# Kernel optimization log

Hardware: AMD Instinct MI355X
Metric: run time of the kernel (lower is better)

Reference implementation:

```python
import jax, jax.numpy as jnp
import numpy as np

D_MODEL = 1024
NUM_HEADS = 16
D_K = D_MODEL // NUM_HEADS


def setup_inputs() -> dict:
    key = jax.random.key(0)
    ks = jax.random.split(key, 8)
    B, S = 2, 2048
    query = jax.random.normal(ks[0], (B, S, D_MODEL), dtype=jnp.float32)
    k_in = jax.random.normal(ks[1], (B, S, D_MODEL), dtype=jnp.float32)
    value = jax.random.normal(ks[2], (B, S, D_MODEL), dtype=jnp.float32)
    # causal mask: True = masked out (upper triangle above diagonal)
    mask = jnp.triu(jnp.ones((S, S), dtype=bool), k=1)[None, None, :, :]
    scale = 1.0 / np.sqrt(D_MODEL)
    W_q = jax.random.normal(ks[3], (D_MODEL, D_MODEL), dtype=jnp.float32) * scale
    W_k = jax.random.normal(ks[4], (D_MODEL, D_MODEL), dtype=jnp.float32) * scale
    W_v = jax.random.normal(ks[5], (D_MODEL, D_MODEL), dtype=jnp.float32) * scale
    W_o = jax.random.normal(ks[6], (D_MODEL, D_MODEL), dtype=jnp.float32) * scale
    return {"query": query, "key": k_in, "value": value, "mask": mask,
            "W_q": W_q, "W_k": W_k, "W_v": W_v, "W_o": W_o}


def _split(x):
    # [B, S, d_model] -> [B, h, S, d_k]
    B, S, _ = x.shape
    return x.reshape(B, S, NUM_HEADS, D_K).transpose(0, 2, 1, 3)


def reference(query, key, value, mask, W_q, W_k, W_v, W_o):
    # torch nn.Linear(bias=False): y = x @ W.T
    Q = _split(query @ W_q.T)   # [B, h, Sq, d_k]
    K = _split(key @ W_k.T)     # [B, h, Sk, d_k]
    V = _split(value @ W_v.T)   # [B, h, Sk, d_k]
    scores = jnp.einsum('bhqd,bhkd->bhqk', Q, K) / jnp.sqrt(jnp.float32(D_K))
    scores = jnp.where(mask, -jnp.inf, scores)
    attn_w = jax.nn.softmax(scores, axis=-1)
    attn_w = jnp.nan_to_num(attn_w, nan=0.0)
    out = jnp.einsum('bhqk,bhkd->bhqd', attn_w, V)  # [B, h, Sq, d_k]
    B, _, Sq, _ = out.shape
    merged = out.transpose(0, 2, 1, 3).reshape(B, Sq, D_MODEL)
    return merged @ W_o.T
```

## Files before the change

kernel.cpp:

```cpp
#include <hip/hip_runtime.h>
#include <hip/hip_bf16.h>
#include <stdint.h>

typedef __attribute__((ext_vector_type(4))) float f32x4;
typedef __attribute__((ext_vector_type(8))) __bf16 bf16x8;
typedef __attribute__((ext_vector_type(4))) unsigned short us4;

#define SEQ 2048
#define DMODEL 1024
#define NH 16
#define DK 64
#define MTOT 4096

__device__ __forceinline__ unsigned short f2bf(float x) {
  union { float f; unsigned int u; } v; v.f = x;
  unsigned int r = v.u + 0x7fffu + ((v.u >> 16) & 1u);
  return (unsigned short)(r >> 16);
}

__device__ __forceinline__ unsigned int cvtpk(float lo, float hi) {
  unsigned int r;
  asm("v_cvt_pk_bf16_f32 %0, %1, %2" : "=v"(r) : "v"(lo), "v"(hi));
  return r;
}

__device__ __forceinline__ f32x4 mfma_bf16(bf16x8 a, bf16x8 b, f32x4 c) {
  return __builtin_amdgcn_mfma_f32_16x16x32_bf16(a, b, c, 0, 0, 0);
}

__device__ __forceinline__ void gload16(const unsigned short* g, unsigned short* l) {
  __builtin_amdgcn_global_load_lds((__attribute__((address_space(1))) void*)g,
                                   (__attribute__((address_space(3))) void*)l,
                                   16, 0, 0);
}

__global__ void cvt_all(const float* __restrict__ s0, const float* __restrict__ s1,
                        const float* __restrict__ s2, const float* __restrict__ s3,
                        const float* __restrict__ s4, const float* __restrict__ s5,
                        const float* __restrict__ s6,
                        unsigned short* __restrict__ d0, unsigned short* __restrict__ d1,
                        unsigned short* __restrict__ d2, unsigned short* __restrict__ d3,
                        unsigned short* __restrict__ d4, unsigned short* __restrict__ d5,
                        unsigned short* __restrict__ d6) {
  const int y = blockIdx.y;
  const float* s = y == 0 ? s0 : y == 1 ? s1 : y == 2 ? s2 : y == 3 ? s3
                 : y == 4 ? s4 : y == 5 ? s5 : s6;
  unsigned short* d = y == 0 ? d0 : y == 1 ? d1 : y == 2 ? d2 : y == 3 ? d3
                    : y == 4 ? d4 : y == 5 ? d5 : d6;
  const int n4 = (y < 3) ? (MTOT * DMODEL / 4) : (DMODEL * DMODEL / 4);
  const int stride = gridDim.x * blockDim.x;
  for (int i = blockIdx.x * blockDim.x + threadIdx.x; i < n4; i += stride) {
    f32x4 v = reinterpret_cast<const f32x4*>(s)[i];
    us4 o;
    o.x = f2bf(v.x); o.y = f2bf(v.y); o.z = f2bf(v.z); o.w = f2bf(v.w);
    reinterpret_cast<us4*>(d)[i] = o;
  }
}

__global__ __launch_bounds__(256) void gemm_qkv(
    const unsigned short* __restrict__ xq, const unsigned short* __restrict__ xk,
    const unsigned short* __restrict__ xv, const unsigned short* __restrict__ bwq,
    const unsigned short* __restrict__ bwk, const unsigned short* __restrict__ bwv,
    unsigned short* __restrict__ Qh, unsigned short* __restrict__ Kh,
    unsigned short* __restrict__ Vt) {
  const int z = blockIdx.z;
  const unsigned short* A = z == 0 ? xq : (z == 1 ? xk : xv);
  const unsigned short* B = z == 0 ? bwq : (z == 1 ? bwk : bwv);
  const float scale = z == 0 ? 0.18033688011112042f : 1.0f;

  __shared__ __align__(16) unsigned short lA[128 * 32];
  __shared__ __align__(16) unsigned short lB[128 * 32];
  const int tid = threadIdx.x;
  const int lane = tid & 63;
  const int wid = tid >> 6;
  const int l15 = lane & 15, l4 = lane >> 4;
  const int bm = blockIdx.x, bn = blockIdx.y;
  const int wr = wid >> 1, wc = wid & 1;

  f32x4 acc[4][4] = {};

  const int chunk0 = (wid * 2 + 0) * 64 + lane;
  const int chunk1 = (wid * 2 + 1) * 64 + lane;
  const unsigned short* gA0 = A + (size_t)(bm * 128 + (chunk0 >> 2)) * 1024 + (chunk0 & 3) * 8;
  const unsigned short* gA1 = A + (size_t)(bm * 128 + (chunk1 >> 2)) * 1024 + (chunk1 & 3) * 8;
  const unsigned short* gB0 = B + (size_t)(bn * 128 + (chunk0 >> 2)) * 1024 + (chunk0 & 3) * 8;
  const unsigned short* gB1 = B + (size_t)(bn * 128 + (chunk1 >> 2)) * 1024 + (chunk1 & 3) * 8;
  unsigned short* lA0 = lA + (wid * 2 + 0) * 512;
  unsigned short* lA1 = lA + (wid * 2 + 1) * 512;
  unsigned short* lB0 = lB + (wid * 2 + 0) * 512;
  unsigned short* lB1 = lB + (wid * 2 + 1) * 512;

  for (int kt = 0; kt < 1024; kt += 32) {
    __syncthreads();
    gload16(gA0 + kt, lA0);
    gload16(gA1 + kt, lA1);
    gload16(gB0 + kt, lB0);
    gload16(gB1 + kt, lB1);
    __syncthreads();
    bf16x8 af[4], bfr[4];
#pragma unroll
    for (int i = 0; i < 4; ++i)
      af[i] = *reinterpret_cast<const bf16x8*>(&lA[(wr * 64 + i * 16 + l15) * 32 + l4 * 8]);
#pragma unroll
    for (int j = 0; j < 4; ++j)
      bfr[j] = *reinterpret_cast<const bf16x8*>(&lB[(wc * 64 + j * 16 + l15) * 32 + l4 * 8]);
    if (z < 2) {
#pragma unroll
      for (int i = 0; i < 4; ++i)
#pragma unroll
        for (int j = 0; j < 4; ++j)
          acc[i][j] = mfma_bf16(bfr[j], af[i], acc[i][j]);
    } else {
#pragma unroll
      for (int i = 0; i < 4; ++i)
#pragma unroll
        for (int j = 0; j < 4; ++j)
          acc[i][j] = mfma_bf16(af[i], bfr[j], acc[i][j]);
    }
  }

  const int row0 = bm * 128 + wr * 64;
  const int col0 = bn * 128 + wc * 64;

  if (z < 2) {
    unsigned short* out = z ? Kh : Qh;
#pragma unroll
    for (int i = 0; i < 4; ++i) {
      const int m = row0 + i * 16 + l15;
      const int b = m >> 11, s = m & 2047;
#pragma unroll
      for (int j = 0; j < 4; ++j) {
        const int n0 = col0 + j * 16 + l4 * 4;
        const int h = n0 >> 6, dd = n0 & 63;
        union { us4 h4; unsigned int u[2]; } pk;
        pk.u[0] = cvtpk(acc[i][j][0] * scale, acc[i][j][1] * scale);
        pk.u[1] = cvtpk(acc[i][j][2] * scale, acc[i][j][3] * scale);
        *reinterpret_cast<us4*>(&out[(size_t)(b * NH + h) * (SEQ * DK) + s * DK + dd]) = pk.h4;
      }
    }
  } else {
#pragma unroll
    for (int i = 0; i < 4; ++i) {
      const int m0 = row0 + i * 16 + l4 * 4;
      const int b = m0 >> 11, s0 = m0 & 2047;
      const int g = (s0 >> 2) & 7;
      const int col = (s0 & ~31) + ((g & 3) << 3) + ((g >> 2) << 2);
#pragma unroll
      for (int j = 0; j < 4; ++j) {
        const int n = col0 + j * 16 + l15;
        const int h = n >> 6, dd = n & 63;
        union { us4 h4; unsigned int u[2]; } pk;
        pk.u[0] = cvtpk(acc[i][j][0], acc[i][j][1]);
        pk.u[1] = cvtpk(acc[i][j][2], acc[i][j][3]);
        *reinterpret_cast<us4*>(&Vt[(size_t)(b * NH + h) * (DK * SEQ) + dd * SEQ + col]) = pk.h4;
      }
    }
  }
}

__global__ __launch_bounds__(512) void gemm_o(const unsigned short* __restrict__ A,
                                              const unsigned short* __restrict__ B,
                                              float* __restrict__ out) {
  __shared__ __align__(16) unsigned short lA3[3][128 * 64];
  __shared__ __align__(16) unsigned short lB3[3][128 * 64];

  const int tid = threadIdx.x;
  const int lane = tid & 63, wid = tid >> 6;
  const int l15 = lane & 15, l4 = lane >> 4;
  const int bm = blockIdx.x, bn = blockIdx.y;
  const int wr = wid >> 1, wc = wid & 1;

  f32x4 acc[2][4] = {};

  const int r8 = lane >> 3, c8 = lane & 7;
  const unsigned short* gAs[2];
  const unsigned short* gBs[2];
  int dstoff[2];
#pragma unroll
  for (int is = 0; is < 2; ++is) {
    const int rbase = is * 64 + wid * 8;
    gAs[is] = A + (size_t)(bm * 128 + rbase + r8) * 1024 + (c8 ^ r8) * 8;
    gBs[is] = B + (size_t)(bn * 128 + rbase + r8) * 1024 + (c8 ^ r8) * 8;
    dstoff[is] = rbase * 64;
  }

#define STAGE_O(t, buf)                                         \
  {                                                             \
    const int kb = (t) * 64;                                    \
    gload16(gAs[0] + kb, &lA3[buf][dstoff[0]]);                 \
    gload16(gAs[1] + kb, &lA3[buf][dstoff[1]]);                 \
    gload16(gBs[0] + kb, &lB3[buf][dstoff[0]]);                 \
    gload16(gBs[1] + kb, &lB3[buf][dstoff[1]]);                 \
  }

  STAGE_O(0, 0);
  STAGE_O(1, 1);

#pragma unroll 1
  for (int t = 0; t < 16; ++t) {
    if (t + 1 < 16) {
      asm volatile("s_waitcnt vmcnt(4)" ::: "memory");
    } else {
      asm volatile("s_waitcnt vmcnt(0)" ::: "memory");
    }
    __builtin_amdgcn_sched_barrier(0);
    __builtin_amdgcn_s_barrier();
    __builtin_amdgcn_sched_barrier(0);

    if (t + 2 < 16) {
      const int pb = (t + 2) % 3;
      STAGE_O(t + 2, pb);
    }

    const unsigned short* La = lA3[t % 3];
    const unsigned short* Lb = lB3[t % 3];
#pragma unroll
    for (int kk = 0; kk < 2; ++kk) {
      bf16x8 af[2], bf[4];
#pragma unroll
      for (int i = 0; i < 2; ++i) {
        const int row = wr * 32 + i * 16 + l15;
        af[i] = *reinterpret_cast<const bf16x8*>(
            &La[row * 64 + (((kk * 4 + l4) ^ (l15 & 7)) * 8)]);
      }
#pragma unroll
      for (int j = 0; j < 4; ++j) {
        const int row = wc * 64 + j * 16 + l15;
        bf[j] = *reinterpret_cast<const bf16x8*>(
            &Lb[row * 64 + (((kk * 4 + l4) ^ (l15 & 7)) * 8)]);
      }
#pragma unroll
      for (int i = 0; i < 2; ++i)
#pragma unroll
        for (int j = 0; j < 4; ++j)
          acc[i][j] = mfma_bf16(bf[j], af[i], acc[i][j]);
    }
  }
#undef STAGE_O

  const int row0 = bm * 128 + wr * 32;
  const int col0 = bn * 128 + wc * 64;
#pragma unroll
  for (int i = 0; i < 2; ++i) {
    const int m = row0 + i * 16 + l15;
#pragma unroll
    for (int j = 0; j < 4; ++j) {
      const int n0 = col0 + j * 16 + l4 * 4;
      *reinterpret_cast<f32x4*>(&out[(size_t)m * DMODEL + n0]) = acc[i][j];
    }
  }
}

__global__ __launch_bounds__(512, 2) void attn_kernel(const unsigned short* __restrict__ Qh,
                                                      const unsigned short* __restrict__ Kh,
                                                      const unsigned short* __restrict__ Vt,
                                                      unsigned short* __restrict__ Mg) {
  __shared__ __align__(16) unsigned short Kl[4][64 * 64];
  __shared__ __align__(16) unsigned short Vl[4][64 * 64];

  const int tid = threadIdx.x;
  const int lane = tid & 63;
  const int w = tid >> 6;
  const int l15 = lane & 15, l4 = lane >> 4;

  const int d = blockIdx.x;
  const int base = d & 255;
  const int pair = d >> 8;
  const int xcd = base & 7;
  const int jj = base >> 3;
  const int bh = (jj >> 3) * 8 + xcd;
  const int qi = jj & 7;
  const int tau = pair ? qi : 15 - qi;

  const unsigned short* Qb = Qh + (size_t)bh * SEQ * DK;
  const unsigned short* Kb = Kh + (size_t)bh * SEQ * DK;
  const unsigned short* Vb = Vt + (size_t)bh * DK * SEQ;
  const int bq = bh >> 4, hh = bh & 15;
  unsigned short* Mbase = Mg + (size_t)bq * SEQ * DMODEL + hh * DK;

  const int srow = lane >> 3;
  const int sswz = (lane & 7) ^ srow;
  const unsigned short* KsrcB = Kb + (size_t)(w * 8 + srow) * DK + sswz * 8;
  const unsigned short* VsrcB = Vb + (size_t)(w * 8 + srow) * SEQ + sswz * 8;

  const int l7 = l15 & 7;

  const int qbase = tau * 128;
  const int q0w = qbase + w * 16;
  const int nt = 2 * tau + 2;

  bf16x8 qf0 = *reinterpret_cast<const bf16x8*>(Qb + (size_t)(q0w + l15) * DK + l4 * 8);
  bf16x8 qf1 = *reinterpret_cast<const bf16x8*>(Qb + (size_t)(q0w + l15) * DK + 32 + l4 * 8);

  f32x4 o[4] = {};
  float mrow = -__builtin_inff();
  float lrow = 0.0f;

  gload16(KsrcB, &Kl[0][w * 512]);
  gload16(VsrcB, &Vl[0][w * 512]);
  gload16(KsrcB + (size_t)64 * DK, &Kl[1][w * 512]);
  gload16(VsrcB + 64, &Vl[1][w * 512]);

  const int S = nt >> 1;
#pragma unroll 1
  for (int s = 0; s < S; ++s) {
    const int t0 = s << 1;
    const int kbase0 = t0 << 6;

    asm volatile("s_waitcnt vmcnt(0)" ::: "memory");
    __builtin_amdgcn_sched_barrier(0);
    __builtin_amdgcn_s_barrier();
    __builtin_amdgcn_sched_barrier(0);

    if (t0 + 2 < nt) {
      gload16(KsrcB + (size_t)(kbase0 + 128) * DK, &Kl[(t0 + 2) & 3][w * 512]);
      gload16(VsrcB + (kbase0 + 128), &Vl[(t0 + 2) & 3][w * 512]);
      gload16(KsrcB + (size_t)(kbase0 + 192) * DK, &Kl[(t0 + 3) & 3][w * 512]);
      gload16(VsrcB + (kbase0 + 192), &Vl[(t0 + 3) & 3][w * 512]);
    }

#pragma unroll
    for (int u = 0; u < 2; ++u) {
      const int t = t0 + u;
      const int kbase = t << 6;
      if (kbase >= q0w + 16) continue;
      const unsigned short* Kc = Kl[t & 3];
      const unsigned short* Vc = Vl[t & 3];

      f32x4 sc[4];
      __builtin_amdgcn_s_setprio(1);
#pragma unroll
      for (int c = 0; c < 4; ++c) {
        const int krow = c * 16 + l15;
        bf16x8 kf0 = *reinterpret_cast<const bf16x8*>(&Kc[krow * 64 + ((l4 ^ l7) * 8)]);
        bf16x8 kf1 = *reinterpret_cast<const bf16x8*>(&Kc[krow * 64 + (((4 + l4) ^ l7) * 8)]);
        f32x4 z = {0.f, 0.f, 0.f, 0.f};
        z = mfma_bf16(kf0, qf0, z);
        sc[c] = mfma_bf16(kf1, qf1, z);
      }
      __builtin_amdgcn_s_setprio(0);

      if (kbase + 63 > q0w) {
        const int qg = q0w + l15;
#pragma unroll
        for (int c = 0; c < 4; ++c) {
          const int kp = kbase + c * 16 + l4 * 4;
#pragma unroll
          for (int r = 0; r < 4; ++r)
            if (kp + r > qg) sc[c][r] = -__builtin_inff();
        }
      }

      f32x4 mv = sc[0];
#pragma unroll
      for (int c = 1; c < 4; ++c)
#pragma unroll
        for (int r = 0; r < 4; ++r) mv[r] = fmaxf(mv[r], sc[c][r]);
      float pm = fmaxf(fmaxf(mv[0], mv[1]), fmaxf(mv[2], mv[3]));
      if (!__all(pm - mrow <= 8.0f)) {
        pm = fmaxf(pm, __shfl_xor(pm, 16));
        pm = fmaxf(pm, __shfl_xor(pm, 32));
        const float mn = fmaxf(mrow, pm);
        const float al = __builtin_amdgcn_exp2f(mrow - mn);
        mrow = mn;
        lrow *= al;
#pragma unroll
        for (int dd = 0; dd < 4; ++dd)
#pragma unroll
          for (int r = 0; r < 4; ++r) o[dd][r] *= al;
      }
      union PB { bf16x8 v; unsigned int u[4]; } pbv[2];
      f32x4 sv = {0.f, 0.f, 0.f, 0.f};
#pragma unroll
      for (int c = 0; c < 4; ++c) {
        const float p0 = __builtin_amdgcn_exp2f(sc[c][0] - mrow);
        const float p1 = __builtin_amdgcn_exp2f(sc[c][1] - mrow);
        const float p2 = __builtin_amdgcn_exp2f(sc[c][2] - mrow);
        const float p3 = __builtin_amdgcn_exp2f(sc[c][3] - mrow);
        sv[0] += p0; sv[1] += p1; sv[2] += p2; sv[3] += p3;
        pbv[c >> 1].u[(c & 1) * 2 + 0] = cvtpk(p0, p1);
        pbv[c >> 1].u[(c & 1) * 2 + 1] = cvtpk(p2, p3);
      }
      lrow += (sv[0] + sv[1]) + (sv[2] + sv[3]);

      __builtin_amdgcn_s_setprio(1);
#pragma unroll
      for (int dd = 0; dd < 4; ++dd) {
        const int vrow = dd * 16 + l15;
#pragma unroll
        for (int p = 0; p < 2; ++p) {
          const bf16x8 av = *reinterpret_cast<const bf16x8*>(
              &Vc[vrow * 64 + (((p * 4 + l4) ^ l7) * 8)]);
          o[dd] = mfma_bf16(av, pbv[p].v, o[dd]);
        }
      }
      __builtin_amdgcn_s_setprio(0);
    }
  }

  lrow += __shfl_xor(lrow, 16);
  lrow += __shfl_xor(lrow, 32);
  const float inv = __builtin_amdgcn_rcpf(lrow);
  const int s = q0w + l15;
#pragma unroll
  for (int dd = 0; dd < 4; ++dd) {
    union { us4 h; unsigned int u[2]; } pk;
    pk.u[0] = cvtpk(o[dd][0] * inv, o[dd][1] * inv);
    pk.u[1] = cvtpk(o[dd][2] * inv, o[dd][3] * inv);
    *reinterpret_cast<us4*>(&Mbase[(size_t)s * DMODEL + dd * 16 + l4 * 4]) = pk.h;
  }
}

extern "C" void kernel_launch(void* const* d_in, const int* in_sizes, int n_in,
                              void* d_out, int out_size, void* d_ws, size_t ws_size,
                              hipStream_t stream) {
  (void)in_sizes; (void)n_in; (void)out_size;
  if (ws_size < (size_t)64 * (1 << 20)) return;

  const float* q = (const float*)d_in[0];
  const float* k = (const float*)d_in[1];
  const float* v = (const float*)d_in[2];
  const float* wq = (const float*)d_in[4];
  const float* wk = (const float*)d_in[5];
  const float* wv = (const float*)d_in[6];
  const float* wo = (const float*)d_in[7];

  char* ws = (char*)d_ws;
  unsigned short* xq  = (unsigned short*)(ws + (size_t)0  * (1 << 20));
  unsigned short* xk  = (unsigned short*)(ws + (size_t)8  * (1 << 20));
  unsigned short* xv  = (unsigned short*)(ws + (size_t)16 * (1 << 20));
  unsigned short* bwq = (unsigned short*)(ws + (size_t)24 * (1 << 20));
  unsigned short* bwk = (unsigned short*)(ws + (size_t)26 * (1 << 20));
  unsigned short* bwv = (unsigned short*)(ws + (size_t)28 * (1 << 20));
  unsigned short* bwo = (unsigned short*)(ws + (size_t)30 * (1 << 20));
  unsigned short* Qh  = (unsigned short*)(ws + (size_t)32 * (1 << 20));
  unsigned short* Kh  = (unsigned short*)(ws + (size_t)40 * (1 << 20));
  unsigned short* Vt  = (unsigned short*)(ws + (size_t)48 * (1 << 20));
  unsigned short* Mg  = (unsigned short*)(ws + (size_t)56 * (1 << 20));

  cvt_all<<<dim3(512, 7), 256, 0, stream>>>(q, k, v, wq, wk, wv, wo,
                                            xq, xk, xv, bwq, bwk, bwv, bwo);
  gemm_qkv<<<dim3(32, 8, 3), 256, 0, stream>>>(xq, xk, xv, bwq, bwk, bwv, Qh, Kh, Vt);
  attn_kernel<<<dim3(512), 512, 0, stream>>>(Qh, Kh, Vt, Mg);
  gemm_o<<<dim3(32, 8), 512, 0, stream>>>(Mg, bwo, (float*)d_out);
}
```

Baseline: 119.8 us.

## Fuse fp32-to-bf16 activation conversion into QKV GEMM tile loads with swizzled LDS

```diff
diff --git a/kernel.cpp b/kernel.cpp
--- a/kernel.cpp
+++ b/kernel.cpp
@@ -28,26 +28,20 @@
   return __builtin_amdgcn_mfma_f32_16x16x32_bf16(a, b, c, 0, 0, 0);
 }
 
-__device__ __forceinline__ void gload16(const unsigned short* g, unsigned short* l) {
-  __builtin_amdgcn_global_load_lds((__attribute__((address_space(1))) void*)g,
+__device__ __forceinline__ void gload16(const void* g, void* l) {
+  __builtin_amdgcn_global_load_lds((const __attribute__((address_space(1))) void*)g,
                                    (__attribute__((address_space(3))) void*)l,
                                    16, 0, 0);
 }
 
-__global__ void cvt_all(const float* __restrict__ s0, const float* __restrict__ s1,
-                        const float* __restrict__ s2, const float* __restrict__ s3,
-                        const float* __restrict__ s4, const float* __restrict__ s5,
-                        const float* __restrict__ s6,
-                        unsigned short* __restrict__ d0, unsigned short* __restrict__ d1,
-                        unsigned short* __restrict__ d2, unsigned short* __restrict__ d3,
-                        unsigned short* __restrict__ d4, unsigned short* __restrict__ d5,
-                        unsigned short* __restrict__ d6) {
+__global__ void cvt_w(const float* __restrict__ s0, const float* __restrict__ s1,
+                      const float* __restrict__ s2, const float* __restrict__ s3,
+                      unsigned short* __restrict__ d0, unsigned short* __restrict__ d1,
+                      unsigned short* __restrict__ d2, unsigned short* __restrict__ d3) {
   const int y = blockIdx.y;
-  const float* s = y == 0 ? s0 : y == 1 ? s1 : y == 2 ? s2 : y == 3 ? s3
-                 : y == 4 ? s4 : y == 5 ? s5 : s6;
-  unsigned short* d = y == 0 ? d0 : y == 1 ? d1 : y == 2 ? d2 : y == 3 ? d3
-                    : y == 4 ? d4 : y == 5 ? d5 : d6;
-  const int n4 = (y < 3) ? (MTOT * DMODEL / 4) : (DMODEL * DMODEL / 4);
+  const float* s = y == 0 ? s0 : y == 1 ? s1 : y == 2 ? s2 : s3;
+  unsigned short* d = y == 0 ? d0 : y == 1 ? d1 : y == 2 ? d2 : d3;
+  const int n4 = DMODEL * DMODEL / 4;
   const int stride = gridDim.x * blockDim.x;
   for (int i = blockIdx.x * blockDim.x + threadIdx.x; i < n4; i += stride) {
     f32x4 v = reinterpret_cast<const f32x4*>(s)[i];
@@ -58,18 +52,18 @@
 }
 
 __global__ __launch_bounds__(256) void gemm_qkv(
-    const unsigned short* __restrict__ xq, const unsigned short* __restrict__ xk,
-    const unsigned short* __restrict__ xv, const unsigned short* __restrict__ bwq,
-    const unsigned short* __restrict__ bwk, const unsigned short* __restrict__ bwv,
+    const float* __restrict__ xq, const float* __restrict__ xk, const float* __restrict__ xv,
+    const unsigned short* __restrict__ bwq, const unsigned short* __restrict__ bwk,
+    const unsigned short* __restrict__ bwv,
     unsigned short* __restrict__ Qh, unsigned short* __restrict__ Kh,
     unsigned short* __restrict__ Vt) {
   const int z = blockIdx.z;
-  const unsigned short* A = z == 0 ? xq : (z == 1 ? xk : xv);
+  const float* A = z == 0 ? xq : (z == 1 ? xk : xv);
   const unsigned short* B = z == 0 ? bwq : (z == 1 ? bwk : bwv);
   const float scale = z == 0 ? 0.18033688011112042f : 1.0f;
 
-  __shared__ __align__(16) unsigned short lA[128 * 32];
-  __shared__ __align__(16) unsigned short lB[128 * 32];
+  __shared__ __align__(16) float lAf[128 * 32];
+  __shared__ __align__(16) unsigned short lB[64 * 64];
   const int tid = threadIdx.x;
   const int lane = tid & 63;
   const int wid = tid >> 6;
@@ -79,31 +73,57 @@
 
   f32x4 acc[4][4] = {};
 
-  const int chunk0 = (wid * 2 + 0) * 64 + lane;
-  const int chunk1 = (wid * 2 + 1) * 64 + lane;
-  const unsigned short* gA0 = A + (size_t)(bm * 128 + (chunk0 >> 2)) * 1024 + (chunk0 & 3) * 8;
-  const unsigned short* gA1 = A + (size_t)(bm * 128 + (chunk1 >> 2)) * 1024 + (chunk1 & 3) * 8;
-  const unsigned short* gB0 = B + (size_t)(bn * 128 + (chunk0 >> 2)) * 1024 + (chunk0 & 3) * 8;
-  const unsigned short* gB1 = B + (size_t)(bn * 128 + (chunk1 >> 2)) * 1024 + (chunk1 & 3) * 8;
-  unsigned short* lA0 = lA + (wid * 2 + 0) * 512;
-  unsigned short* lA1 = lA + (wid * 2 + 1) * 512;
-  unsigned short* lB0 = lB + (wid * 2 + 0) * 512;
-  unsigned short* lB1 = lB + (wid * 2 + 1) * 512;
+  const float* gAsrc[4];
+  float* lAdst[4];
+#pragma unroll
+  for (int is = 0; is < 4; ++is) {
+    const int G = is * 256 + tid;
+    const int row = G >> 3, pp = G & 7;
+    const int lg = pp ^ (row & 7);
+    gAsrc[is] = A + (size_t)(bm * 128 + row) * 1024 + lg * 4;
+    lAdst[is] = lAf + (is * 256 + wid * 64) * 4;
+  }
+  const unsigned short* gBsrc[2];
+  unsigned short* lBdst[2];
+#pragma unroll
+  for (int is = 0; is < 2; ++is) {
+    const int G = is * 256 + tid;
+    const int sr = G >> 3, pp = G & 7;
+    const int lg = pp ^ (sr & 7);
+    const int row = sr * 2 + (lg >> 2), kc = lg & 3;
+    gBsrc[is] = B + (size_t)(bn * 128 + row) * 1024 + kc * 8;
+    lBdst[is] = lB + (is * 256 + wid * 64) * 8;
+  }
 
   for (int kt = 0; kt < 1024; kt += 32) {
     __syncthreads();
-    gload16(gA0 + kt, lA0);
-    gload16(gA1 + kt, lA1);
-    gload16(gB0 + kt, lB0);
-    gload16(gB1 + kt, lB1);
+#pragma unroll
+    for (int is = 0; is < 4; ++is) gload16(gAsrc[is] + kt, lAdst[is]);
+#pragma unroll
+    for (int is = 0; is < 2; ++is) gload16(gBsrc[is] + kt, lBdst[is]);
     __syncthreads();
+
     bf16x8 af[4], bfr[4];
 #pragma unroll
-    for (int i = 0; i < 4; ++i)
-      af[i] = *reinterpret_cast<const bf16x8*>(&lA[(wr * 64 + i * 16 + l15) * 32 + l4 * 8]);
-#pragma unroll
-    for (int j = 0; j < 4; ++j)
-      bfr[j] = *reinterpret_cast<const bf16x8*>(&lB[(wc * 64 + j * 16 + l15) * 32 + l4 * 8]);
+    for (int i = 0; i < 4; ++i) {
+      const int row = wr * 64 + i * 16 + l15;
+      const int rb = row * 32, rx = row & 7;
+      const f32x4 v0 = *reinterpret_cast<const f32x4*>(&lAf[rb + (((2 * l4 + 0) ^ rx) * 4)]);
+      const f32x4 v1 = *reinterpret_cast<const f32x4*>(&lAf[rb + (((2 * l4 + 1) ^ rx) * 4)]);
+      union { bf16x8 v; unsigned int u[4]; } t;
+      t.u[0] = cvtpk(v0.x, v0.y);
+      t.u[1] = cvtpk(v0.z, v0.w);
+      t.u[2] = cvtpk(v1.x, v1.y);
+      t.u[3] = cvtpk(v1.z, v1.w);
+      af[i] = t.v;
+    }
+#pragma unroll
+    for (int j = 0; j < 4; ++j) {
+      const int row = wc * 64 + j * 16 + l15;
+      const int sr = row >> 1;
+      const int pp = (((row & 1) << 2) | l4) ^ (sr & 7);
+      bfr[j] = *reinterpret_cast<const bf16x8*>(&lB[sr * 64 + pp * 8]);
+    }
     if (z < 2) {
 #pragma unroll
       for (int i = 0; i < 4; ++i)
@@ -426,9 +446,6 @@
   const float* wo = (const float*)d_in[7];
 
   char* ws = (char*)d_ws;
-  unsigned short* xq  = (unsigned short*)(ws + (size_t)0  * (1 << 20));
-  unsigned short* xk  = (unsigned short*)(ws + (size_t)8  * (1 << 20));
-  unsigned short* xv  = (unsigned short*)(ws + (size_t)16 * (1 << 20));
   unsigned short* bwq = (unsigned short*)(ws + (size_t)24 * (1 << 20));
   unsigned short* bwk = (unsigned short*)(ws + (size_t)26 * (1 << 20));
   unsigned short* bwv = (unsigned short*)(ws + (size_t)28 * (1 << 20));
@@ -438,9 +455,8 @@
   unsigned short* Vt  = (unsigned short*)(ws + (size_t)48 * (1 << 20));
   unsigned short* Mg  = (unsigned short*)(ws + (size_t)56 * (1 << 20));
 
-  cvt_all<<<dim3(512, 7), 256, 0, stream>>>(q, k, v, wq, wk, wv, wo,
-                                            xq, xk, xv, bwq, bwk, bwv, bwo);
-  gemm_qkv<<<dim3(32, 8, 3), 256, 0, stream>>>(xq, xk, xv, bwq, bwk, bwv, Qh, Kh, Vt);
+  cvt_w<<<dim3(64, 4), 256, 0, stream>>>(wq, wk, wv, wo, bwq, bwk, bwv, bwo);
+  gemm_qkv<<<dim3(32, 8, 3), 256, 0, stream>>>(q, k, v, bwq, bwk, bwv, Qh, Kh, Vt);
   attn_kernel<<<dim3(512), 512, 0, stream>>>(Qh, Kh, Vt, Mg);
   gemm_o<<<dim3(32, 8), 512, 0, stream>>>(Mg, bwo, (float*)d_out);
 }
```

Result: slower. 133.5 us (+11.5%).

## Pipeline QKV GEMM with triple-buffered LDS, swizzled layout and 512 threads

Applied to the files above, without the earlier changes.

```diff
diff --git a/kernel.cpp b/kernel.cpp
--- a/kernel.cpp
+++ b/kernel.cpp
@@ -57,7 +57,7 @@
   }
 }
 
-__global__ __launch_bounds__(256) void gemm_qkv(
+__global__ __launch_bounds__(512) void gemm_qkv(
     const unsigned short* __restrict__ xq, const unsigned short* __restrict__ xk,
     const unsigned short* __restrict__ xv, const unsigned short* __restrict__ bwq,
     const unsigned short* __restrict__ bwk, const unsigned short* __restrict__ bwv,
@@ -68,64 +68,98 @@
   const unsigned short* B = z == 0 ? bwq : (z == 1 ? bwk : bwv);
   const float scale = z == 0 ? 0.18033688011112042f : 1.0f;
 
-  __shared__ __align__(16) unsigned short lA[128 * 32];
-  __shared__ __align__(16) unsigned short lB[128 * 32];
+  __shared__ __align__(16) unsigned short lA3[3][128 * 64];
+  __shared__ __align__(16) unsigned short lB3[3][128 * 64];
+
   const int tid = threadIdx.x;
-  const int lane = tid & 63;
-  const int wid = tid >> 6;
+  const int lane = tid & 63, wid = tid >> 6;
   const int l15 = lane & 15, l4 = lane >> 4;
   const int bm = blockIdx.x, bn = blockIdx.y;
   const int wr = wid >> 1, wc = wid & 1;
 
-  f32x4 acc[4][4] = {};
-
-  const int chunk0 = (wid * 2 + 0) * 64 + lane;
-  const int chunk1 = (wid * 2 + 1) * 64 + lane;
-  const unsigned short* gA0 = A + (size_t)(bm * 128 + (chunk0 >> 2)) * 1024 + (chunk0 & 3) * 8;
-  const unsigned short* gA1 = A + (size_t)(bm * 128 + (chunk1 >> 2)) * 1024 + (chunk1 & 3) * 8;
-  const unsigned short* gB0 = B + (size_t)(bn * 128 + (chunk0 >> 2)) * 1024 + (chunk0 & 3) * 8;
-  const unsigned short* gB1 = B + (size_t)(bn * 128 + (chunk1 >> 2)) * 1024 + (chunk1 & 3) * 8;
-  unsigned short* lA0 = lA + (wid * 2 + 0) * 512;
-  unsigned short* lA1 = lA + (wid * 2 + 1) * 512;
-  unsigned short* lB0 = lB + (wid * 2 + 0) * 512;
-  unsigned short* lB1 = lB + (wid * 2 + 1) * 512;
-
-  for (int kt = 0; kt < 1024; kt += 32) {
-    __syncthreads();
-    gload16(gA0 + kt, lA0);
-    gload16(gA1 + kt, lA1);
-    gload16(gB0 + kt, lB0);
-    gload16(gB1 + kt, lB1);
-    __syncthreads();
-    bf16x8 af[4], bfr[4];
-#pragma unroll
-    for (int i = 0; i < 4; ++i)
-      af[i] = *reinterpret_cast<const bf16x8*>(&lA[(wr * 64 + i * 16 + l15) * 32 + l4 * 8]);
-#pragma unroll
-    for (int j = 0; j < 4; ++j)
-      bfr[j] = *reinterpret_cast<const bf16x8*>(&lB[(wc * 64 + j * 16 + l15) * 32 + l4 * 8]);
-    if (z < 2) {
-#pragma unroll
-      for (int i = 0; i < 4; ++i)
-#pragma unroll
-        for (int j = 0; j < 4; ++j)
-          acc[i][j] = mfma_bf16(bfr[j], af[i], acc[i][j]);
+  f32x4 acc[2][4] = {};
+
+  const int r8 = lane >> 3, c8 = lane & 7;
+  const unsigned short* gAs[2];
+  const unsigned short* gBs[2];
+  int dstoff[2];
+#pragma unroll
+  for (int is = 0; is < 2; ++is) {
+    const int rbase = is * 64 + wid * 8;
+    gAs[is] = A + (size_t)(bm * 128 + rbase + r8) * 1024 + (c8 ^ r8) * 8;
+    gBs[is] = B + (size_t)(bn * 128 + rbase + r8) * 1024 + (c8 ^ r8) * 8;
+    dstoff[is] = rbase * 64;
+  }
+
+#define STAGE_P(t, buf)                                         \
+  {                                                             \
+    const int kb = (t) * 64;                                    \
+    gload16(gAs[0] + kb, &lA3[buf][dstoff[0]]);                 \
+    gload16(gAs[1] + kb, &lA3[buf][dstoff[1]]);                 \
+    gload16(gBs[0] + kb, &lB3[buf][dstoff[0]]);                 \
+    gload16(gBs[1] + kb, &lB3[buf][dstoff[1]]);                 \
+  }
+
+  STAGE_P(0, 0);
+  STAGE_P(1, 1);
+
+#pragma unroll 1
+  for (int t = 0; t < 16; ++t) {
+    if (t + 1 < 16) {
+      asm volatile("s_waitcnt vmcnt(4)" ::: "memory");
     } else {
-#pragma unroll
-      for (int i = 0; i < 4; ++i)
-#pragma unroll
-        for (int j = 0; j < 4; ++j)
-          acc[i][j] = mfma_bf16(af[i], bfr[j], acc[i][j]);
-    }
-  }
-
-  const int row0 = bm * 128 + wr * 64;
+      asm volatile("s_waitcnt vmcnt(0)" ::: "memory");
+    }
+    __builtin_amdgcn_sched_barrier(0);
+    __builtin_amdgcn_s_barrier();
+    __builtin_amdgcn_sched_barrier(0);
+
+    if (t + 2 < 16) {
+      const int pb = (t + 2) % 3;
+      STAGE_P(t + 2, pb);
+    }
+
+    const unsigned short* La = lA3[t % 3];
+    const unsigned short* Lb = lB3[t % 3];
+#pragma unroll
+    for (int kk = 0; kk < 2; ++kk) {
+      bf16x8 af[2], bf[4];
+#pragma unroll
+      for (int i = 0; i < 2; ++i) {
+        const int row = wr * 32 + i * 16 + l15;
+        af[i] = *reinterpret_cast<const bf16x8*>(
+            &La[row * 64 + (((kk * 4 + l4) ^ (l15 & 7)) * 8)]);
+      }
+#pragma unroll
+      for (int j = 0; j < 4; ++j) {
+        const int row = wc * 64 + j * 16 + l15;
+        bf[j] = *reinterpret_cast<const bf16x8*>(
+            &Lb[row * 64 + (((kk * 4 + l4) ^ (l15 & 7)) * 8)]);
+      }
+      if (z < 2) {
+#pragma unroll
+        for (int i = 0; i < 2; ++i)
+#pragma unroll
+          for (int j = 0; j < 4; ++j)
+            acc[i][j] = mfma_bf16(bf[j], af[i], acc[i][j]);
+      } else {
+#pragma unroll
+        for (int i = 0; i < 2; ++i)
+#pragma unroll
+          for (int j = 0; j < 4; ++j)
+            acc[i][j] = mfma_bf16(af[i], bf[j], acc[i][j]);
+      }
+    }
+  }
+#undef STAGE_P
+
+  const int row0 = bm * 128 + wr * 32;
   const int col0 = bn * 128 + wc * 64;
 
   if (z < 2) {
     unsigned short* out = z ? Kh : Qh;
 #pragma unroll
-    for (int i = 0; i < 4; ++i) {
+    for (int i = 0; i < 2; ++i) {
       const int m = row0 + i * 16 + l15;
       const int b = m >> 11, s = m & 2047;
 #pragma unroll
@@ -140,7 +174,7 @@
     }
   } else {
 #pragma unroll
-    for (int i = 0; i < 4; ++i) {
+    for (int i = 0; i < 2; ++i) {
       const int m0 = row0 + i * 16 + l4 * 4;
       const int b = m0 >> 11, s0 = m0 & 2047;
       const int g = (s0 >> 2) & 7;
@@ -440,7 +474,7 @@
 
   cvt_all<<<dim3(512, 7), 256, 0, stream>>>(q, k, v, wq, wk, wv, wo,
                                             xq, xk, xv, bwq, bwk, bwv, bwo);
-  gemm_qkv<<<dim3(32, 8, 3), 256, 0, stream>>>(xq, xk, xv, bwq, bwk, bwv, Qh, Kh, Vt);
+  gemm_qkv<<<dim3(32, 8, 3), 512, 0, stream>>>(xq, xk, xv, bwq, bwk, bwv, Qh, Kh, Vt);
   attn_kernel<<<dim3(512), 512, 0, stream>>>(Qh, Kh, Vt, Mg);
   gemm_o<<<dim3(32, 8), 512, 0, stream>>>(Mg, bwo, (float*)d_out);
 }
```

Result: slower. 124.1 us (+3.6%).
